# Kernel optimization log

Hardware: AMD Instinct MI355X
Metric: run time of the kernel (lower is better)

## Reference

```python
import jax, jax.numpy as jnp
from jax import lax
import numpy as np

N, T, U = 8, 300, 60
E_ENC, E_DEC, NHID, VOCAB, BLANK = 320, 320, 512, 128, 0


def setup_inputs() -> dict:
    key = jax.random.key(0)
    ks = jax.random.split(key, 6)
    enc_state = jax.random.normal(ks[0], (N, T, E_ENC), jnp.float32)
    dec_state = jax.random.normal(ks[1], (N, U + 1, E_DEC), jnp.float32)
    targets = jax.random.randint(ks[2], (N, U), 1, VOCAB, jnp.int32)  # non-blank labels
    inputs_len = jnp.full((N,), T, jnp.int32)
    targets_len = jnp.full((N,), U, jnp.int32)
    W_joint = jax.random.normal(ks[3], (E_ENC + E_DEC, NHID), jnp.float32) * (1.0 / np.sqrt(E_ENC + E_DEC))
    b_joint = jnp.zeros((NHID,), jnp.float32)
    W_out = jax.random.normal(ks[4], (NHID, VOCAB), jnp.float32) * (1.0 / np.sqrt(NHID))
    b_out = jnp.zeros((VOCAB,), jnp.float32)
    return dict(enc_state=enc_state, dec_state=dec_state, targets=targets,
                inputs_len=inputs_len, targets_len=targets_len,
                W_joint=W_joint, b_joint=b_joint, W_out=W_out, b_out=b_out)


def _joint_log_probs(enc, dec, Wj, bj, Wo, bo):
    # Original: broadcast enc [N,T,1,Ee] + dec [N,1,U1,Ed], concat, Linear, Tanh, Linear, log_softmax.
    # Splitting W_joint over the concat axis is exactly equivalent and avoids the [N,T,U1,Ee+Ed] tensor.
    Ee = enc.shape[-1]
    h = (jnp.einsum('nte,eh->nth', enc, Wj[:Ee])[:, :, None, :]
         + jnp.einsum('nue,eh->nuh', dec, Wj[Ee:])[:, None, :, :]
         + bj)                                              # [N,T,U1,NHID]
    logits = jnp.einsum('ntuh,hv->ntuv', jnp.tanh(h), Wo) + bo  # [N,T,U1,V]
    return jax.nn.log_softmax(logits, axis=-1)


def _rnnt_loss(logp, targets, inputs_len, targets_len, blank):
    # Forward (alpha) DP over the T x (U+1) lattice, vectorized over batch.
    Nb, Tt, U1, V = logp.shape
    blank_lp = logp[..., blank]                                        # [N,T,U1]
    emit_lp = jnp.take_along_axis(logp[:, :, :U1 - 1, :],
                                  targets[:, None, :, None], axis=-1)[..., 0]  # [N,T,U]
    # Row t=0: alpha[0,u] = sum_{u'<u} emit[0,u'].
    a0 = jnp.concatenate([jnp.zeros((Nb, 1), logp.dtype),
                          jnp.cumsum(emit_lp[:, 0, :], axis=1)], axis=1)       # [N,U1]

    def row_step(prev, xs):
        blank_tm1, emit_t = xs                      # [N,U1], [N,U]
        base = prev + blank_tm1                     # path arriving from (t-1,u) via blank

        def u_step(carry, xs_u):
            b_u, e_u = xs_u                         # [N], [N]
            v = jnp.logaddexp(b_u, carry + e_u)     # blank-from-below vs emit-from-left
            return v, v

        _, rest = lax.scan(u_step, base[:, 0], (base[:, 1:].T, emit_t.T))      # [U,N]
        row = jnp.concatenate([base[:, :1], rest.T], axis=1)                   # [N,U1]
        return row, row

    _, rows = lax.scan(row_step, a0,
                       (jnp.swapaxes(blank_lp[:, :-1], 0, 1),
                        jnp.swapaxes(emit_lp[:, 1:], 0, 1)))                   # [T-1,N,U1]
    alpha = jnp.concatenate([a0[:, None, :], jnp.swapaxes(rows, 0, 1)], axis=1)  # [N,T,U1]

    ti = (inputs_len - 1).astype(jnp.int32)
    ui = targets_len.astype(jnp.int32)
    n = jnp.arange(Nb)
    log_p = alpha[n, ti, ui] + blank_lp[n, ti, ui]  # final blank transition
    return -log_p


def reference(enc_state, dec_state, targets, inputs_len, targets_len,
              W_joint, b_joint, W_out, b_out):
    logp = _joint_log_probs(enc_state, dec_state, W_joint, b_joint, W_out, b_out)
    loss = _rnnt_loss(logp, targets, inputs_len, targets_len, BLANK)
    return loss.mean()
```

## Files before the change

kernel.cpp:

```cpp
#include <hip/hip_runtime.h>
#include <hip/hip_bf16.h>
#include <hip/hip_fp16.h>

#define N_   8
#define T_   300
#define U_   60
#define U1_  61
#define EENC 320
#define NHID 512
#define VOC  128
#define SKROWS 384
#define INV_LN2 1.4426950408889634f
#define LN2 0.6931471805599453f
#define SCALE2 2.8853900817779268f

typedef __attribute__((ext_vector_type(8))) short bf16x8;
typedef __attribute__((ext_vector_type(4))) float f32x4;

__device__ __forceinline__ unsigned short f2bf(float f) {
    unsigned int u = __float_as_uint(f);
    u += 0x7fff + ((u >> 16) & 1);
    return (unsigned short)(u >> 16);
}

__device__ __forceinline__ float lae2(float x, float y) {
    float m = fmaxf(x, y);
    float d = fminf(fabsf(x - y), 1e30f);
    return m + log2f(1.f + exp2f(-d));
}

__device__ __forceinline__ float4 gload16(const void* p) {
    float4 v;
    asm volatile("global_load_dwordx4 %0, %1, off" : "=v"(v) : "v"(p) : "memory");
    return v;
}
#define WAITVM(n) __builtin_amdgcn_s_waitcnt(0x0F70 | (n))

__global__ __launch_bounds__(256) void convert_w(
    const float* __restrict__ Wj, const float* __restrict__ Wo,
    unsigned short* __restrict__ WjT, unsigned short* __restrict__ WoT2,
    float* __restrict__ bosum)
{
    __shared__ float tile[32][33];
    int bid = blockIdx.x;
    const float* S; unsigned short* D; int k0, c0, K, C; bool isWo;
    if (bid < 160) { S = Wj; D = WjT; K = 320; C = 512; k0 = (bid >> 4) * 32; c0 = (bid & 15) * 32; isWo = false; }
    else { bid -= 160; S = Wo; D = WoT2; K = 512; C = 128; k0 = (bid >> 2) * 32; c0 = (bid & 3) * 32; isWo = true; }
    const int tx = threadIdx.x & 31, ty = threadIdx.x >> 5;
    float part = 0.f;
    #pragma unroll
    for (int i = 0; i < 32; i += 8) {
        float v = S[(k0 + ty + i) * C + c0 + tx];
        tile[ty + i][tx] = v;
        part += v;
    }
    __syncthreads();
    const float mulf = isWo ? -2.f : 1.f;
    #pragma unroll
    for (int i = 0; i < 32; i += 8)
        D[(c0 + ty + i) * K + k0 + tx] = f2bf(mulf * tile[tx][ty + i]);
    if (isWo) atomicAdd(&bosum[c0 + tx], part);
}

__global__ __launch_bounds__(256) void proj_mfma(
    const float* __restrict__ Xe, const float* __restrict__ Xd,
    const unsigned short* __restrict__ BT,
    const float* __restrict__ bj,
    float* __restrict__ Ce, float* __restrict__ Cd)
{
    __shared__ short lA[64 * 64];
    __shared__ short lB[128 * 64];
    int bid = blockIdx.x;
    const float* X; float* Cp; const float* bias; int R;
    if (bid < 152) { X = Xe; Cp = Ce; bias = nullptr; R = N_ * T_; }
    else { bid -= 152; X = Xd; Cp = Cd; bias = bj; R = N_ * U1_; }
    const int tid = threadIdx.x, lane = tid & 63, wave = tid >> 6;
    const int rb = bid >> 2, cb = bid & 3;
    const int rh = wave & 1, ch = wave >> 1;
    const int sr = tid >> 3, sg = tid & 7;
    const int frow = lane & 15, fg = lane >> 4, quad = lane >> 4;

    f32x4 acc[2][4];
    f32x4 z = {0.f, 0.f, 0.f, 0.f};
    #pragma unroll
    for (int a = 0; a < 2; ++a)
        #pragma unroll
        for (int b = 0; b < 4; ++b) acc[a][b] = z;

    for (int s = 0; s < 5; ++s) {
        __syncthreads();
        #pragma unroll
        for (int p = 0; p < 2; ++p) {
            int row = sr + p * 32;
            int grow = rb * 64 + row; if (grow >= R) grow = R - 1;
            const float* xp = X + grow * EENC + s * 64 + sg * 8;
            float4 x0 = *(const float4*)xp, x1 = *(const float4*)(xp + 4);
            bf16x8 va;
            va[0] = (short)f2bf(x0.x); va[1] = (short)f2bf(x0.y);
            va[2] = (short)f2bf(x0.z); va[3] = (short)f2bf(x0.w);
            va[4] = (short)f2bf(x1.x); va[5] = (short)f2bf(x1.y);
            va[6] = (short)f2bf(x1.z); va[7] = (short)f2bf(x1.w);
            *(bf16x8*)&lA[row * 64 + ((sg ^ (row & 7)) << 3)] = va;
        }
        #pragma unroll
        for (int p = 0; p < 4; ++p) {
            int col = sr + p * 32;
            bf16x8 vb = *(const bf16x8*)(BT + (cb * 128 + col) * EENC + s * 64 + sg * 8);
            *(bf16x8*)&lB[col * 64 + ((sg ^ (col & 7)) << 3)] = vb;
        }
        __syncthreads();
        #pragma unroll
        for (int ks = 0; ks < 2; ++ks) {
            int g = fg + ks * 4;
            bf16x8 af[2], bf[4];
            #pragma unroll
            for (int rt = 0; rt < 2; ++rt) {
                int row = rh * 32 + rt * 16 + frow;
                af[rt] = *(const bf16x8*)&lA[row * 64 + ((g ^ (row & 7)) << 3)];
            }
            #pragma unroll
            for (int c = 0; c < 4; ++c) {
                int col = ch * 64 + c * 16 + frow;
                bf[c] = *(const bf16x8*)&lB[col * 64 + ((g ^ (col & 7)) << 3)];
            }
            #pragma unroll
            for (int rt = 0; rt < 2; ++rt)
                #pragma unroll
                for (int c = 0; c < 4; ++c)
                    acc[rt][c] = __builtin_amdgcn_mfma_f32_16x16x32_bf16(af[rt], bf[c], acc[rt][c], 0, 0, 0);
        }
    }
    #pragma unroll
    for (int rt = 0; rt < 2; ++rt) {
        int grow0 = rb * 64 + rh * 32 + rt * 16 + quad * 4;
        #pragma unroll
        for (int c = 0; c < 4; ++c) {
            int col = cb * 128 + ch * 64 + c * 16 + frow;
            float b = bias ? bias[col] : 0.f;
            #pragma unroll
            for (int r = 0; r < 4; ++r) {
                int gr = grow0 + r;
                if (gr < R) Cp[gr * NHID + col] = (acc[rt][c][r] + b) * SCALE2;
            }
        }
    }
}

__global__ __launch_bounds__(512, 4) void joint_mfma(
    const float* __restrict__ encp,
    const float* __restrict__ decp,
    const unsigned short* __restrict__ WoT2,
    const float* __restrict__ bo, const float* __restrict__ bosum,
    const int* __restrict__ targets,
    unsigned short* __restrict__ Zs)
{
    __shared__ short lA[256 * 64];
    __shared__ short lB[128 * 64];
    __shared__ float bo_s[VOC];
    __shared__ int   lab_s[U_];

    const int tid = threadIdx.x, lane = tid & 63, wave = tid >> 6;
    const int nt0 = 4 * blockIdx.x, n = nt0 / T_;
    const int t0 = nt0 - n * T_;
    if (tid < VOC) bo_s[tid] = bo[tid] + bosum[tid];
    else if (tid < VOC + U_) lab_s[tid - VOC] = targets[n * U_ + (tid - VOC)];

    const int frow = lane & 15, quad = lane >> 4;
    const int sg = tid & 7, sr = tid >> 3;

    f32x4 acc[2][8];
    f32x4 z = {0.f, 0.f, 0.f, 0.f};
    #pragma unroll
    for (int rt = 0; rt < 2; ++rt)
        #pragma unroll
        for (int c = 0; c < 8; ++c) acc[rt][c] = z;

    const int ua = min(sr, U_);
    const float* dbase = decp + (size_t)(n * U1_ + ua) * NHID + sg * 8;
    const float* ebase = encp + (size_t)nt0 * NHID + sg * 8;

    for (int s = 0; s < 8; ++s) {
        __syncthreads();
        #pragma unroll
        for (int p = 0; p < 2; ++p) {
            int col = sr + p * 64;
            bf16x8 vb = *(const bf16x8*)(WoT2 + col * NHID + s * 64 + sg * 8);
            *(bf16x8*)&lB[col * 64 + ((sg ^ (col & 7)) << 3)] = vb;
        }
        const float* dp = dbase + s * 64;
        float4 d0 = *(const float4*)dp, d1 = *(const float4*)(dp + 4);
        #pragma unroll
        for (int p = 0; p < 4; ++p) {
            const float* ep = ebase + (size_t)p * NHID + s * 64;
            float4 e0 = *(const float4*)ep, e1 = *(const float4*)(ep + 4);
            float s0 = __builtin_amdgcn_rcpf(__builtin_amdgcn_exp2f(e0.x + d0.x) + 1.f);
            float s1 = __builtin_amdgcn_rcpf(__builtin_amdgcn_exp2f(e0.y + d0.y) + 1.f);
            float s2 = __builtin_amdgcn_rcpf(__builtin_amdgcn_exp2f(e0.z + d0.z) + 1.f);
            float s3 = __builtin_amdgcn_rcpf(__builtin_amdgcn_exp2f(e0.w + d0.w) + 1.f);
            float s4 = __builtin_amdgcn_rcpf(__builtin_amdgcn_exp2f(e1.x + d1.x) + 1.f);
            float s5 = __builtin_amdgcn_rcpf(__builtin_amdgcn_exp2f(e1.y + d1.y) + 1.f);
            float s6 = __builtin_amdgcn_rcpf(__builtin_amdgcn_exp2f(e1.z + d1.z) + 1.f);
            float s7 = __builtin_amdgcn_rcpf(__builtin_amdgcn_exp2f(e1.w + d1.w) + 1.f);
            unsigned b0 = __float_as_uint(s0) + 0x8000u, b1 = __float_as_uint(s1) + 0x8000u;
            unsigned b2 = __float_as_uint(s2) + 0x8000u, b3 = __float_as_uint(s3) + 0x8000u;
            unsigned b4 = __float_as_uint(s4) + 0x8000u, b5 = __float_as_uint(s5) + 0x8000u;
            unsigned b6 = __float_as_uint(s6) + 0x8000u, b7 = __float_as_uint(s7) + 0x8000u;
            union { unsigned u4[4]; bf16x8 v; } va;
            va.u4[0] = __builtin_amdgcn_perm(b1, b0, 0x07060302);
            va.u4[1] = __builtin_amdgcn_perm(b3, b2, 0x07060302);
            va.u4[2] = __builtin_amdgcn_perm(b5, b4, 0x07060302);
            va.u4[3] = __builtin_amdgcn_perm(b7, b6, 0x07060302);
            int row = sr + p * 64;
            *(bf16x8*)&lA[row * 64 + ((sg ^ (row & 7)) << 3)] = va.v;
        }
        __syncthreads();
        #pragma unroll
        for (int ks = 0; ks < 2; ++ks) {
            const int g = ks * 4 + quad;
            bf16x8 af[2];
            #pragma unroll
            for (int rt = 0; rt < 2; ++rt) {
                int ar = wave * 32 + rt * 16 + frow;
                af[rt] = *(const bf16x8*)&lA[ar * 64 + ((g ^ (ar & 7)) << 3)];
            }
            #pragma unroll
            for (int c = 0; c < 8; ++c) {
                int col = c * 16 + frow;
                const bf16x8 bfr = *(const bf16x8*)&lB[col * 64 + ((g ^ (col & 7)) << 3)];
                acc[0][c] = __builtin_amdgcn_mfma_f32_16x16x32_bf16(af[0], bfr, acc[0][c], 0, 0, 0);
                acc[1][c] = __builtin_amdgcn_mfma_f32_16x16x32_bf16(af[1], bfr, acc[1][c], 0, 0, 0);
            }
        }
    }

    #pragma unroll
    for (int rt = 0; rt < 2; ++rt) {
        #pragma unroll
        for (int c = 0; c < 8; ++c) {
            float b = bo_s[c * 16 + frow];
            #pragma unroll
            for (int r = 0; r < 4; ++r) acc[rt][c][r] += b;
        }
        float mx[4], sm[4];
        #pragma unroll
        for (int r = 0; r < 4; ++r) {
            float m = acc[rt][0][r];
            #pragma unroll
            for (int c = 1; c < 8; ++c) m = fmaxf(m, acc[rt][c][r]);
            mx[r] = m;
        }
        #pragma unroll
        for (int off = 1; off < 16; off <<= 1)
            #pragma unroll
            for (int r = 0; r < 4; ++r) mx[r] = fmaxf(mx[r], __shfl_xor(mx[r], off));
        #pragma unroll
        for (int r = 0; r < 4; ++r) {
            float ss = 0.f;
            #pragma unroll
            for (int c = 0; c < 8; ++c) ss += __expf(acc[rt][c][r] - mx[r]);
            sm[r] = ss;
        }
        #pragma unroll
        for (int off = 1; off < 16; off <<= 1)
            #pragma unroll
            for (int r = 0; r < 4; ++r) sm[r] += __shfl_xor(sm[r], off);

        #pragma unroll
        for (int r = 0; r < 4; ++r) {
            float lse = mx[r] + __logf(sm[r]);
            int row = wave * 32 + rt * 16 + quad * 4 + r;
            int urow = row & 63, ntl = row >> 6;
            size_t rowz = (size_t)(n * SKROWS + t0 + ntl + urow + 1) * 64;
            if (urow < U1_ && frow == 0) {
                __half hh = __float2half_rn((acc[rt][0][r] - lse) * INV_LN2);
                Zs[(rowz + urow) * 2] = __half_as_ushort(hh);
            }
            if (urow < U_) {
                int lab = lab_s[urow];
                if (frow == (lab & 15)) {
                    int cw = lab >> 4;
                    float pick = acc[rt][0][r];
                    #pragma unroll
                    for (int c = 1; c < 8; ++c) if (c == cw) pick = acc[rt][c][r];
                    __half hh = __float2half_rn((pick - lse) * INV_LN2);
                    Zs[(rowz + urow + 1) * 2 + 1] = __half_as_ushort(hh);
                }
            }
        }
    }
}

__global__ __launch_bounds__(512) void dp_kernel(
    const unsigned* __restrict__ Z,
    const int* __restrict__ inputs_len, const int* __restrict__ targets_len,
    float* __restrict__ out)
{
    __shared__ float losses[N_];
    __shared__ float guard;
    const int tid = threadIdx.x;
    if (tid >= 128) {
        const float4* W = (const float4*)Z;
        float acc = 0.f;
        const int nv = N_ * SKROWS * 16;
        for (int i = tid - 128; i < nv; i += 384) acc += W[i].x;
        if (__float_as_uint(acc) == 0x7F123456u) guard = acc;
    } else {
        const int n  = tid >> 4;
        const int c  = tid & 15;
        const int u0 = c * 4;
        const char* Zn = (const char*)(Z + (size_t)n * SKROWS * 64) + u0 * 4;
        const unsigned len_t = (unsigned)inputs_len[n];
        const int ui = targets_len[n];
        const int ti = (int)len_t - 1;
        const bool u_is0 = (c == 0);

        float a0 = u_is0 ? 0.f : -1e30f;
        float a1 = -1e30f, a2 = -1e30f, a3 = -1e30f;

        float4 zq[8];
        #pragma unroll
        for (int j = 0; j < 8; ++j) zq[j] = gload16(Zn + (size_t)(1 + j) * 256);

        for (int d0 = 1; d0 < 361; d0 += 8) {
            #pragma unroll
            for (int j = 0; j < 8; ++j) {
                const int d = d0 + j;
                WAITVM(7);
                float4 zv = zq[j];
                zq[j] = gload16(Zn + (size_t)(d + 8) * 256);
                const __half2* hz = (const __half2*)&zv;
                float2 w0 = __half22float2(hz[0]);
                float2 w1 = __half22float2(hz[1]);
                float2 w2 = __half22float2(hz[2]);
                float2 w3 = __half22float2(hz[3]);
                float av0 = __shfl_up(a3, 1);
                float e0 = u_is0 ? -1e30f : w0.y;
                float n0 = lae2(a0 + w0.x, av0 + e0);
                float n1 = lae2(a1 + w1.x, a0 + w1.y);
                float n2 = lae2(a2 + w2.x, a1 + w2.y);
                float n3 = lae2(a3 + w3.x, a2 + w3.y);
                a0 = ((unsigned)(d - u0)     < len_t) ? n0 : a0;
                a1 = ((unsigned)(d - u0 - 1) < len_t) ? n1 : a1;
                a2 = ((unsigned)(d - u0 - 2) < len_t) ? n2 : a2;
                a3 = ((unsigned)(d - u0 - 3) < len_t) ? n3 : a3;
            }
        }
        WAITVM(0);
        float av[4] = {a0, a1, a2, a3};
        #pragma unroll
        for (int j = 0; j < 4; ++j)
            if (u0 + j == ui) {
                const __half2* hf = (const __half2*)((const char*)(Z + (size_t)n * SKROWS * 64)
                                                     + ((size_t)(ti + ui + 1) * 64 + ui) * 4);
                float blf = __half22float2(hf[0]).x;
                losses[n] = -(av[j] + blf) * LN2;
            }
    }
    __syncthreads();
    if (tid == 0) {
        float s = 0.f;
        #pragma unroll
        for (int i = 0; i < N_; ++i) s += losses[i];
        out[0] = s * (1.0f / N_);
    }
}

extern "C" void kernel_launch(void* const* d_in, const int* in_sizes, int n_in,
                              void* d_out, int out_size, void* d_ws, size_t ws_size,
                              hipStream_t stream)
{
    const float* enc         = (const float*)d_in[0];
    const float* dec         = (const float*)d_in[1];
    const int*   targets     = (const int*)d_in[2];
    const int*   inputs_len  = (const int*)d_in[3];
    const int*   targets_len = (const int*)d_in[4];
    const float* Wj          = (const float*)d_in[5];
    const float* bj          = (const float*)d_in[6];
    const float* Wo          = (const float*)d_in[7];
    const float* bo          = (const float*)d_in[8];
    float* out = (float*)d_out;

    char* ws = (char*)d_ws;
    float*          encp  = (float*)(ws + 0);
    float*          decp  = (float*)(ws + 4915200);
    unsigned*       Z     = (unsigned*)(ws + 5914624);
    unsigned short* WjT   = (unsigned short*)(ws + 6701056);
    unsigned short* WoT2  = (unsigned short*)(ws + 7028736);
    float*          bosum = (float*)(ws + 7159872);

    hipMemsetAsync(bosum, 0, VOC * sizeof(float), stream);
    convert_w<<<224, 256, 0, stream>>>(Wj, Wo, WjT, WoT2, bosum);
    proj_mfma<<<184, 256, 0, stream>>>(enc, dec, WjT, bj, encp, decp);
    joint_mfma<<<600, 512, 0, stream>>>(encp, decp, WoT2, bo, bosum, targets, (unsigned short*)Z);
    dp_kernel<<<1, 512, 0, stream>>>(Z, inputs_len, targets_len, out);
}
```

Baseline: 213.4 us.

## Map one lattice column per thread in DP kernel and drop cache-warming threads

The anti-diagonal DP kernel now gives each batch item a full 64-lane wavefront with one u column per lane, instead of 16 lanes each owning four columns. Each step does one logaddexp per lane, which shortens the serial dependency chain per diagonal, and prefetches 16 diagonals deep with dword loads. The extra threads that swept Z to warm the cache are removed, so loads may see more latency. It also adds a cross-lane shuffle on every column.

```diff
diff --git a/kernel.cpp b/kernel.cpp
--- a/kernel.cpp
+++ b/kernel.cpp
@@ -29,12 +29,11 @@
     return m + log2f(1.f + exp2f(-d));
 }
 
-__device__ __forceinline__ float4 gload16(const void* p) {
-    float4 v;
-    asm volatile("global_load_dwordx4 %0, %1, off" : "=v"(v) : "v"(p) : "memory");
+__device__ __forceinline__ unsigned gload4(const void* p) {
+    unsigned v;
+    asm volatile("global_load_dword %0, %1, off" : "=v"(v) : "v"(p) : "memory");
     return v;
 }
-#define WAITVM(n) __builtin_amdgcn_s_waitcnt(0x0F70 | (n))
 
 __global__ __launch_bounds__(256) void convert_w(
     const float* __restrict__ Wj, const float* __restrict__ Wo,
@@ -296,65 +295,48 @@
     float* __restrict__ out)
 {
     __shared__ float losses[N_];
-    __shared__ float guard;
     const int tid = threadIdx.x;
-    if (tid >= 128) {
-        const float4* W = (const float4*)Z;
-        float acc = 0.f;
-        const int nv = N_ * SKROWS * 16;
-        for (int i = tid - 128; i < nv; i += 384) acc += W[i].x;
-        if (__float_as_uint(acc) == 0x7F123456u) guard = acc;
-    } else {
-        const int n  = tid >> 4;
-        const int c  = tid & 15;
-        const int u0 = c * 4;
-        const char* Zn = (const char*)(Z + (size_t)n * SKROWS * 64) + u0 * 4;
-        const unsigned len_t = (unsigned)inputs_len[n];
-        const int ui = targets_len[n];
-        const int ti = (int)len_t - 1;
-        const bool u_is0 = (c == 0);
-
-        float a0 = u_is0 ? 0.f : -1e30f;
-        float a1 = -1e30f, a2 = -1e30f, a3 = -1e30f;
-
-        float4 zq[8];
-        #pragma unroll
-        for (int j = 0; j < 8; ++j) zq[j] = gload16(Zn + (size_t)(1 + j) * 256);
-
-        for (int d0 = 1; d0 < 361; d0 += 8) {
-            #pragma unroll
-            for (int j = 0; j < 8; ++j) {
-                const int d = d0 + j;
-                WAITVM(7);
-                float4 zv = zq[j];
-                zq[j] = gload16(Zn + (size_t)(d + 8) * 256);
-                const __half2* hz = (const __half2*)&zv;
-                float2 w0 = __half22float2(hz[0]);
-                float2 w1 = __half22float2(hz[1]);
-                float2 w2 = __half22float2(hz[2]);
-                float2 w3 = __half22float2(hz[3]);
-                float av0 = __shfl_up(a3, 1);
-                float e0 = u_is0 ? -1e30f : w0.y;
-                float n0 = lae2(a0 + w0.x, av0 + e0);
-                float n1 = lae2(a1 + w1.x, a0 + w1.y);
-                float n2 = lae2(a2 + w2.x, a1 + w2.y);
-                float n3 = lae2(a3 + w3.x, a2 + w3.y);
-                a0 = ((unsigned)(d - u0)     < len_t) ? n0 : a0;
-                a1 = ((unsigned)(d - u0 - 1) < len_t) ? n1 : a1;
-                a2 = ((unsigned)(d - u0 - 2) < len_t) ? n2 : a2;
-                a3 = ((unsigned)(d - u0 - 3) < len_t) ? n3 : a3;
-            }
-        }
-        WAITVM(0);
-        float av[4] = {a0, a1, a2, a3};
-        #pragma unroll
-        for (int j = 0; j < 4; ++j)
-            if (u0 + j == ui) {
-                const __half2* hf = (const __half2*)((const char*)(Z + (size_t)n * SKROWS * 64)
-                                                     + ((size_t)(ti + ui + 1) * 64 + ui) * 4);
-                float blf = __half22float2(hf[0]).x;
-                losses[n] = -(av[j] + blf) * LN2;
-            }
+    const int n = tid >> 6;
+    const int u = tid & 63;
+    const bool u_is0 = (u == 0);
+
+    const unsigned len_t = (unsigned)inputs_len[n];
+    const int ui = targets_len[n];
+    const int ti = (int)len_t - 1;
+
+    const char* Zn = (const char*)(Z + (size_t)n * SKROWS * 64) + u * 4;
+
+    float a = u_is0 ? 0.f : -1e30f;
+
+    unsigned zq[16];
+    #pragma unroll
+    for (int j = 0; j < 16; ++j) zq[j] = gload4(Zn + (size_t)(1 + j) * 256);
+
+    for (int d0 = 1; d0 < 361; d0 += 16) {
+        const char* pn = Zn + (size_t)(d0 + 16) * 256;
+        #pragma unroll
+        for (int j = 0; j < 16; ++j) {
+            const int d = d0 + j;
+            asm volatile("s_waitcnt vmcnt(15)");
+            asm volatile("" : "+v"(zq[j]));
+            unsigned zv = zq[j];
+            zq[j] = gload4(pn + (size_t)j * 256);
+            union { unsigned u32; __half2 h2; } cv; cv.u32 = zv;
+            float2 w = __half22float2(cv.h2);
+            float av = __shfl_up(a, 1);
+            float b  = a + w.x;
+            float e  = av + (u_is0 ? -1e30f : w.y);
+            float nn = lae2(b, e);
+            a = ((unsigned)(d - u) < len_t) ? nn : a;
+        }
+    }
+
+    if (u == ui) {
+        const unsigned* Zb = Z + (size_t)n * SKROWS * 64;
+        unsigned wf = Zb[(size_t)(ti + ui + 1) * 64 + ui];
+        union { unsigned u32; __half2 h2; } cf; cf.u32 = wf;
+        float blf = __half22float2(cf.h2).x;
+        losses[n] = -(a + blf) * LN2;
     }
     __syncthreads();
     if (tid == 0) {
```

Measured after the change: 188.3 us. -11.8%, faster.
